# Kernel optimization log

Hardware: AMD Instinct MI355X
Metric: run time of the kernel (lower is better)

The kernel has to match this reference:

```python
import jax, jax.numpy as jnp
import numpy as np

PNUM = 128
BATCH = 8192


def setup_inputs() -> dict:
    key = jax.random.key(0)
    k0, k1, k2 = jax.random.split(key, 3)
    return {
        "pred0": jax.random.normal(k0, (BATCH, PNUM, 2), dtype=jnp.float32),
        "pred1": jax.random.normal(k1, (BATCH, PNUM, 2), dtype=jnp.float32),
        "gt": jax.random.normal(k2, (BATCH, PNUM, 2), dtype=jnp.float32),
    }


def _smooth_l1(d):
    # F.smooth_l1_loss with default beta=1.0, reduction='none'
    a = jnp.abs(d)
    return jnp.where(a < 1.0, 0.5 * d * d, a - 0.5)


def _match_loss(pred, gt):
    # pred, gt: [B, pnum, 2]
    pnum = pred.shape[1]
    # cyclic index: idx[i, j] = (i + j) % pnum  (row i = gt rolled by i)
    idx = (jnp.arange(pnum)[:, None] + jnp.arange(pnum)[None, :]) % pnum
    gt_expand = gt[:, idx]                      # [B, pnum, pnum, 2]
    diff = pred[:, None, :, :] - gt_expand      # broadcast pred over shift dim i
    dis = _smooth_l1(diff).sum(-1).mean(axis=2)  # [B, pnum] mean over vertices j
    return jnp.min(dis, axis=1)                  # min over cyclic shift i -> [B]


def reference(pred0, pred1, gt):
    loss = _match_loss(pred0, gt).mean() + _match_loss(pred1, gt).mean()
    return loss / 2.0
```

## Files before the change

### kernel.cpp

```cpp
#include <hip/hip_runtime.h>
#include <stdint.h>

#define PNUM 128
#define BATCH 8192
#define WPB 4
#define GRID1 (BATCH / WPB)

typedef uint32_t u32;
typedef uint32_t u32x2 __attribute__((ext_vector_type(2)));
typedef uint32_t u32x4 __attribute__((ext_vector_type(4)));

__device__ __forceinline__ u32 cvt2u(float x, float y) {
    return __builtin_bit_cast(u32, __builtin_amdgcn_cvt_pkrtz(x, y));
}

__device__ __forceinline__ void unit(u32 p, u32 q, float& acc, u32 cOne, u32 cNegHalf) {
    u32 d, a, m, t;
    asm("v_pk_add_f16 %0, %1, %2 neg_lo:[0,1] neg_hi:[0,1]" : "=v"(d) : "v"(p), "v"(q));
    asm("v_and_b32 %0, 0x7fff7fff, %1" : "=v"(a) : "v"(d));
    asm("v_pk_min_f16 %0, %1, %2" : "=v"(m) : "v"(a), "v"(cOne));
    asm("v_pk_fma_f16 %0, %1, %2, %3" : "=v"(t) : "v"(m), "v"(cNegHalf), "v"(a));
    asm("v_dot2_f32_f16 %0, %1, %2, %0" : "+v"(acc) : "v"(m), "v"(t));
}

#define DSR64(dst, addr, OFF) \
    asm volatile("ds_read_b64 %0, %1 offset:" OFF : "=v"(dst) : "v"(addr))
#define DSR128(dst, addr, OFF) \
    asm volatile("ds_read_b128 %0, %1 offset:" OFF : "=v"(dst) : "v"(addr))
#define WAITLG(N) \
    asm volatile("s_waitcnt lgkmcnt(" #N ")" ::: "memory"); \
    __builtin_amdgcn_sched_barrier(0)

#define COMPUTE(naC, nbC, q0C, q1C, Wv) \
    unit(q0C[0], Wv[0],  a00, cOne, cNegHalf); \
    unit(q0C[1], Wv[1],  a00, cOne, cNegHalf); \
    unit(q0C[2], naC[0], a00, cOne, cNegHalf); \
    unit(q0C[3], naC[1], a00, cOne, cNegHalf); \
    unit(q0C[0], Wv[1],  a01, cOne, cNegHalf); \
    unit(q0C[1], naC[0], a01, cOne, cNegHalf); \
    unit(q0C[2], naC[1], a01, cOne, cNegHalf); \
    unit(q0C[3], nbC[0], a01, cOne, cNegHalf); \
    unit(q1C[0], Wv[0],  a10, cOne, cNegHalf); \
    unit(q1C[1], Wv[1],  a10, cOne, cNegHalf); \
    unit(q1C[2], naC[0], a10, cOne, cNegHalf); \
    unit(q1C[3], naC[1], a10, cOne, cNegHalf); \
    unit(q1C[0], Wv[1],  a11, cOne, cNegHalf); \
    unit(q1C[1], naC[0], a11, cOne, cNegHalf); \
    unit(q1C[2], naC[1], a11, cOne, cNegHalf); \
    unit(q1C[3], nbC[0], a11, cOne, cNegHalf)

__global__ __launch_bounds__(64 * WPB, 8) void match_fused(
        const float* __restrict__ pred0,
        const float* __restrict__ pred1,
        const float* __restrict__ gt,
        float* __restrict__ ws) {
    __shared__ __align__(16) _Float16 lds[WPB][1024];
    __shared__ float bsum[WPB];

    const int t = threadIdx.x;
    const int k = t & 63;
    const int w = __builtin_amdgcn_readfirstlane(t >> 6);
    const int b = blockIdx.x * WPB + w;

    _Float16* base = lds[w];
    uint2* ringU = (uint2*)base;
    uint2* q0s   = (uint2*)(base + 512);
    uint2* q1s   = (uint2*)(base + 768);

    const float4* gv4 = (const float4*)(gt    + (size_t)b * (PNUM * 2));
    const float4* p0v = (const float4*)(pred0 + (size_t)b * (PNUM * 2));
    const float4* p1v = (const float4*)(pred1 + (size_t)b * (PNUM * 2));
    {
        float4 g = gv4[k];
        uint2 gh = {cvt2u(g.x, g.y), cvt2u(g.z, g.w)};
        ringU[k] = gh; ringU[k + 64] = gh;
        float4 p = p0v[k];
        q0s[k] = (uint2){cvt2u(p.x, p.y), cvt2u(p.z, p.w)};
        p = p1v[k];
        q1s[k] = (uint2){cvt2u(p.x, p.y), cvt2u(p.z, p.w)};
    }

    u32 ldsb = (u32)(uintptr_t)base;
    u32 gA = ldsb + (u32)(k * 8);
    u32 pA = ldsb + 1024;

    asm volatile("s_waitcnt lgkmcnt(0)" ::: "memory");
    __builtin_amdgcn_sched_barrier(0);

    u32 cOne = 0x3C003C00u;
    u32 cNegHalf = 0xB800B800u;

    u32x2 na0, nb0, na1, nb1, na2, nb2;
    u32x4 q0b0, q1b0, q0b1, q1b1, q0b2, q1b2;

    DSR64(nb2, gA, "0");
    DSR64(na0, gA, "8");   DSR64(nb0, gA, "16");
    DSR128(q0b0, pA, "0"); DSR128(q1b0, pA, "512");
    DSR64(na1, gA, "24");  DSR64(nb1, gA, "32");
    DSR128(q0b1, pA, "16"); DSR128(q1b1, pA, "528");

    float a00 = 0.f, a01 = 0.f, a10 = 0.f, a11 = 0.f;

    for (int bdy = 0; bdy < 10; ++bdy) {
        WAITLG(4);
        COMPUTE(na0, nb0, q0b0, q1b0, nb2);
        DSR64(na2, gA, "40");  DSR64(nb2, gA, "48");
        DSR128(q0b2, pA, "32"); DSR128(q1b2, pA, "544");
        WAITLG(4);
        COMPUTE(na1, nb1, q0b1, q1b1, nb0);
        DSR64(na0, gA, "56");  DSR64(nb0, gA, "64");
        DSR128(q0b0, pA, "48"); DSR128(q1b0, pA, "560");
        WAITLG(4);
        COMPUTE(na2, nb2, q0b2, q1b2, nb1);
        DSR64(na1, gA, "72");  DSR64(nb1, gA, "80");
        DSR128(q0b1, pA, "64"); DSR128(q1b1, pA, "576");
        gA += 48; pA += 48;
    }
    WAITLG(4);
    COMPUTE(na0, nb0, q0b0, q1b0, nb2);
    WAITLG(0);
    COMPUTE(na1, nb1, q0b1, q1b1, nb0);

    float r0 = fminf(a00, a01);
    float r1 = fminf(a10, a11);
#pragma unroll
    for (int m = 32; m > 0; m >>= 1) {
        r0 = fminf(r0, __shfl_xor(r0, m, 64));
        r1 = fminf(r1, __shfl_xor(r1, m, 64));
    }

    if (k == 0) bsum[w] = r0 + r1;
    __syncthreads();
    if (t == 0) {
        ws[blockIdx.x] = bsum[0] + bsum[1] + bsum[2] + bsum[3];
    }
}

__global__ __launch_bounds__(256) void reduce_out(
        const float* __restrict__ ws, float* __restrict__ out) {
    const int t = threadIdx.x;
    const float4* w4 = (const float4*)ws;
    float4 v0 = w4[t];
    float4 v1 = w4[t + 256];
    float s = ((v0.x + v0.y) + (v0.z + v0.w)) + ((v1.x + v1.y) + (v1.z + v1.w));
#pragma unroll
    for (int m = 32; m > 0; m >>= 1) s += __shfl_xor(s, m, 64);
    __shared__ float acc[4];
    const int w = t >> 6;
    if ((t & 63) == 0) acc[w] = s;
    __syncthreads();
    if (t == 0)
        out[0] = (acc[0] + acc[1] + acc[2] + acc[3]) * (1.0f / (2.0f * BATCH * PNUM));
}

extern "C" void kernel_launch(void* const* d_in, const int* in_sizes, int n_in,
                              void* d_out, int out_size, void* d_ws, size_t ws_size,
                              hipStream_t stream) {
    const float* pred0 = (const float*)d_in[0];
    const float* pred1 = (const float*)d_in[1];
    const float* gt    = (const float*)d_in[2];
    float* out = (float*)d_out;
    float* ws  = (float*)d_ws;

    match_fused<<<GRID1, 64 * WPB, 0, stream>>>(pred0, pred1, gt, ws);
    reduce_out<<<1, 256, 0, stream>>>(ws, out);
}
```

Before: 111.6 us.

## Merge gt LDS reads into ds_read2_b64 and stagger wave start offsets

Replaces the two separate ds_read_b64 gt loads per step with one ds_read2_b64, so fewer LDS instructions are issued and the wait threshold drops. Each wave in a block now starts its walk over vertex chunks at a different offset (w*8) and wraps modulo 32 chunks, so the waves of a block read different LDS regions at the same time. The loop is kept rolled and restructured around a register ring that carries the spill-over words. The risk is added address-wrap arithmetic in the loop and possible LDS bank conflicts from the new read pattern.

```diff
diff --git a/kernel.cpp b/kernel.cpp
--- a/kernel.cpp
+++ b/kernel.cpp
@@ -23,31 +23,40 @@
     asm("v_dot2_f32_f16 %0, %1, %2, %0" : "+v"(acc) : "v"(m), "v"(t));
 }
 
-#define DSR64(dst, addr, OFF) \
-    asm volatile("ds_read_b64 %0, %1 offset:" OFF : "=v"(dst) : "v"(addr))
+#define DSR64(dst, addr) \
+    asm volatile("ds_read_b64 %0, %1" : "=v"(dst) : "v"(addr))
 #define DSR128(dst, addr, OFF) \
     asm volatile("ds_read_b128 %0, %1 offset:" OFF : "=v"(dst) : "v"(addr))
+#define DSR2x64(dst, addr) \
+    asm volatile("ds_read2_b64 %0, %1 offset0:1 offset1:2" : "=v"(dst) : "v"(addr))
 #define WAITLG(N) \
     asm volatile("s_waitcnt lgkmcnt(" #N ")" ::: "memory"); \
     __builtin_amdgcn_sched_barrier(0)
 
-#define COMPUTE(naC, nbC, q0C, q1C, Wv) \
-    unit(q0C[0], Wv[0],  a00, cOne, cNegHalf); \
-    unit(q0C[1], Wv[1],  a00, cOne, cNegHalf); \
-    unit(q0C[2], naC[0], a00, cOne, cNegHalf); \
-    unit(q0C[3], naC[1], a00, cOne, cNegHalf); \
-    unit(q0C[0], Wv[1],  a01, cOne, cNegHalf); \
-    unit(q0C[1], naC[0], a01, cOne, cNegHalf); \
-    unit(q0C[2], naC[1], a01, cOne, cNegHalf); \
-    unit(q0C[3], nbC[0], a01, cOne, cNegHalf); \
-    unit(q1C[0], Wv[0],  a10, cOne, cNegHalf); \
-    unit(q1C[1], Wv[1],  a10, cOne, cNegHalf); \
-    unit(q1C[2], naC[0], a10, cOne, cNegHalf); \
-    unit(q1C[3], naC[1], a10, cOne, cNegHalf); \
-    unit(q1C[0], Wv[1],  a11, cOne, cNegHalf); \
-    unit(q1C[1], naC[0], a11, cOne, cNegHalf); \
-    unit(q1C[2], naC[1], a11, cOne, cNegHalf); \
-    unit(q1C[3], nbC[0], a11, cOne, cNegHalf)
+#define ISSUE(Bg, Bq0, Bq1) \
+    DSR2x64(Bg, issGA); \
+    DSR128(Bq0, issPA, "0"); \
+    DSR128(Bq1, issPA, "512"); \
+    issGA += 16; issPA += 16; \
+    if (++ii == 32) { ii = 0; issGA = gA0; issPA = pA0; }
+
+#define COMPUTE(G, Q0, Q1, W0, W1) \
+    unit(Q0[0], W0,   a00, cOne, cNegHalf); \
+    unit(Q0[1], W1,   a00, cOne, cNegHalf); \
+    unit(Q0[2], G[0], a00, cOne, cNegHalf); \
+    unit(Q0[3], G[1], a00, cOne, cNegHalf); \
+    unit(Q0[0], W1,   a01, cOne, cNegHalf); \
+    unit(Q0[1], G[0], a01, cOne, cNegHalf); \
+    unit(Q0[2], G[1], a01, cOne, cNegHalf); \
+    unit(Q0[3], G[2], a01, cOne, cNegHalf); \
+    unit(Q1[0], W0,   a10, cOne, cNegHalf); \
+    unit(Q1[1], W1,   a10, cOne, cNegHalf); \
+    unit(Q1[2], G[0], a10, cOne, cNegHalf); \
+    unit(Q1[3], G[1], a10, cOne, cNegHalf); \
+    unit(Q1[0], W1,   a11, cOne, cNegHalf); \
+    unit(Q1[1], G[0], a11, cOne, cNegHalf); \
+    unit(Q1[2], G[1], a11, cOne, cNegHalf); \
+    unit(Q1[3], G[2], a11, cOne, cNegHalf)
 
 __global__ __launch_bounds__(64 * WPB, 8) void match_fused(
         const float* __restrict__ pred0,
@@ -80,46 +89,41 @@
         q1s[k] = (uint2){cvt2u(p.x, p.y), cvt2u(p.z, p.w)};
     }
 
-    u32 ldsb = (u32)(uintptr_t)base;
-    u32 gA = ldsb + (u32)(k * 8);
-    u32 pA = ldsb + 1024;
+    const u32 ldsb = (u32)(uintptr_t)base;
+    const u32 gA0 = ldsb + (u32)(k * 8);
+    const u32 pA0 = ldsb + 1024;
 
     asm volatile("s_waitcnt lgkmcnt(0)" ::: "memory");
     __builtin_amdgcn_sched_barrier(0);
 
-    u32 cOne = 0x3C003C00u;
-    u32 cNegHalf = 0xB800B800u;
+    const u32 cOne = 0x3C003C00u;
+    const u32 cNegHalf = 0xB800B800u;
 
-    u32x2 na0, nb0, na1, nb1, na2, nb2;
-    u32x4 q0b0, q1b0, q0b1, q1b1, q0b2, q1b2;
+    const int h0 = w * 8;
+    int ii = h0;
+    u32 issGA = gA0 + (u32)(16 * h0);
+    u32 issPA = pA0 + (u32)(16 * h0);
 
-    DSR64(nb2, gA, "0");
-    DSR64(na0, gA, "8");   DSR64(nb0, gA, "16");
-    DSR128(q0b0, pA, "0"); DSR128(q1b0, pA, "512");
-    DSR64(na1, gA, "24");  DSR64(nb1, gA, "32");
-    DSR128(q0b1, pA, "16"); DSR128(q1b1, pA, "528");
+    u32x2 Wsp;
+    DSR64(Wsp, issGA);
+    u32x4 b0g, b0q0, b0q1, b1g, b1q0, b1q1, b2g, b2q0, b2q1;
+    ISSUE(b0g, b0q0, b0q1);
+    ISSUE(b1g, b1q0, b1q1);
 
     float a00 = 0.f, a01 = 0.f, a10 = 0.f, a11 = 0.f;
 
-    for (int bdy = 0; bdy < 10; ++bdy) {
-        WAITLG(4);
-        COMPUTE(na0, nb0, q0b0, q1b0, nb2);
-        DSR64(na2, gA, "40");  DSR64(nb2, gA, "48");
-        DSR128(q0b2, pA, "32"); DSR128(q1b2, pA, "544");
-        WAITLG(4);
-        COMPUTE(na1, nb1, q0b1, q1b1, nb0);
-        DSR64(na0, gA, "56");  DSR64(nb0, gA, "64");
-        DSR128(q0b0, pA, "48"); DSR128(q1b0, pA, "560");
-        WAITLG(4);
-        COMPUTE(na2, nb2, q0b2, q1b2, nb1);
-        DSR64(na1, gA, "72");  DSR64(nb1, gA, "80");
-        DSR128(q0b1, pA, "64"); DSR128(q1b1, pA, "576");
-        gA += 48; pA += 48;
+    WAITLG(3); COMPUTE(b0g, b0q0, b0q1, Wsp[0], Wsp[1]); ISSUE(b2g, b2q0, b2q1);
+    WAITLG(3); COMPUTE(b1g, b1q0, b1q1, b0g[2], b0g[3]); ISSUE(b0g, b0q0, b0q1);
+    WAITLG(3); COMPUTE(b2g, b2q0, b2q1, b1g[2], b1g[3]); ISSUE(b1g, b1q0, b1q1);
+
+#pragma unroll 1
+    for (int tr = 0; tr < 9; ++tr) {
+        WAITLG(3); COMPUTE(b0g, b0q0, b0q1, b2g[2], b2g[3]); ISSUE(b2g, b2q0, b2q1);
+        WAITLG(3); COMPUTE(b1g, b1q0, b1q1, b0g[2], b0g[3]); ISSUE(b0g, b0q0, b0q1);
+        WAITLG(3); COMPUTE(b2g, b2q0, b2q1, b1g[2], b1g[3]); ISSUE(b1g, b1q0, b1q1);
     }
-    WAITLG(4);
-    COMPUTE(na0, nb0, q0b0, q1b0, nb2);
-    WAITLG(0);
-    COMPUTE(na1, nb1, q0b1, q1b1, nb0);
+    WAITLG(3); COMPUTE(b0g, b0q0, b0q1, b2g[2], b2g[3]);
+    WAITLG(0); COMPUTE(b1g, b1q0, b1q1, b0g[2], b0g[3]);
 
     float r0 = fminf(a00, a01);
     float r1 = fminf(a10, a11);
```

Result: no change. 112.7 us (+1.0%).
